# Kernel tuning notes

Measured on AMD Instinct MI355X. Metric: run time of the kernel, lower is better.

Reference implementation:

```python
import math
import jax, jax.numpy as jnp
import numpy as np

DIM_IN = 2048
DIM_OUT = 2048
BLOCK = 128
N_BLOCKS = 256
SPARSITY = 0.1
BATCH = 8192


def setup_inputs() -> dict:
    key = jax.random.key(0)
    k1, k2, k3, k4, k5 = jax.random.split(key, 5)
    x = jax.random.normal(k1, (BATCH, DIM_IN), dtype=jnp.float32)
    weight = jax.random.normal(k2, (DIM_IN, DIM_OUT), dtype=jnp.float32) * (1.0 / math.sqrt(DIM_IN))
    bias = jax.random.normal(k3, (DIM_OUT,), dtype=jnp.float32) * 0.01
    gate_w = jax.random.normal(k4, (DIM_IN, N_BLOCKS), dtype=jnp.float32) * (1.0 / math.sqrt(DIM_IN))
    gate_b = jax.random.normal(k5, (N_BLOCKS,), dtype=jnp.float32) * 0.01
    return {"x": x, "weight": weight, "bias": bias, "gate_w": gate_w, "gate_b": gate_b}


def _sparsify1d(g):
    # k-th largest kept per row; threshold, mask, renormalize (Sparsify1D)
    n = g.shape[-1]
    k = int(math.ceil(SPARSITY * n))
    topval = jax.lax.top_k(g, k)[0][:, -1:]          # (B, 1) k-th largest value
    res = jnp.where(g >= topval, g, jnp.zeros_like(g))
    return res / (jnp.sum(res, axis=-1, keepdims=True) / n)


def reference(x, weight, bias, gate_w, gate_b):
    B = x.shape[0]
    s = DIM_IN // BLOCK                               # 16 block-rows/cols
    # gate network: Linear -> Sparsify1D
    g = _sparsify1d(x @ gate_w + gate_b)              # (B, s*s)
    gb = g.reshape(B, s, s)                           # (B, s_in, s_out)
    xb = x.reshape(B, s, BLOCK)                       # (B, s_in, block)
    Wb = weight.reshape(s, BLOCK, s, BLOCK)           # (s_in, block, s_out, block)
    # gated block matrix-vector multiply:
    # y[b,q,n] = sum_{p,m} g[b,p,q] * x[b,p,m] * W[p,m,q,n]
    y = jnp.einsum('bpq,bpm,pmqn->bqn', gb, xb, Wb)
    return y.reshape(B, DIM_OUT) + bias
```

## Files before the change

kernel.cpp:

```cpp
#include <hip/hip_runtime.h>
#include <hip/hip_bf16.h>
#include <stdint.h>

#define BATCH  8192
#define DIN    2048
#define DOUT   2048
#define NB     256
#define KSEL   26

typedef __attribute__((ext_vector_type(2))) float f32x2;
typedef __attribute__((ext_vector_type(4))) float f32x4;
typedef __attribute__((ext_vector_type(8))) __bf16 bf16x8;
typedef __attribute__((ext_vector_type(8))) unsigned short u16x8;
typedef __attribute__((ext_vector_type(4))) unsigned short u16x4;

__device__ __forceinline__ float bf2f(unsigned short u){
  union { unsigned int i; float f; } v; v.i = ((unsigned int)u) << 16; return v.f;
}
__device__ __forceinline__ unsigned short f2bf(float f){
  union { float f; unsigned int i; } v; v.f = f;
  unsigned int x = v.i;
  return (unsigned short)((x + 0x7FFFu + ((x >> 16) & 1u)) >> 16);
}
__device__ __forceinline__ unsigned short f2bf_c(float f){
  __bf16 b = (__bf16)f;
  union { __bf16 b; unsigned short u; } v; v.b = b; return v.u;
}

__global__ __launch_bounds__(256) void conv_wt(const float* __restrict__ w, unsigned short* __restrict__ wt)
{
  __shared__ float tl[64][65];
  const int k0 = blockIdx.x * 64;
  const int n0 = blockIdx.y * 64;
  const int c  = threadIdx.x & 63;
  const int r4 = threadIdx.x >> 6;
  #pragma unroll
  for (int i = 0; i < 16; i++){
    const int r = r4 * 16 + i;
    tl[r][c] = w[(size_t)(k0 + r) * DOUT + n0 + c];
  }
  __syncthreads();
  #pragma unroll
  for (int i = 0; i < 16; i++){
    const int n = r4 * 16 + i;
    wt[(size_t)(n0 + n) * DIN + k0 + c] = f2bf(tl[c][n]);
  }
}

__global__ __launch_bounds__(256) void gate_gemm(
    const float* __restrict__ x, const float* __restrict__ gw,
    float* __restrict__ part, unsigned short* __restrict__ xb)
{
  __shared__ float xT[32][36];
  const int b0   = blockIdx.x * 32;
  const int ks   = blockIdx.y;
  const int t    = threadIdx.x;
  const int lane = t & 63;
  const int wv   = t >> 6;
  const int rg   = (wv >> 1) * 16;
  const int cb   = (wv & 1) * 128 + (lane << 1);

  float acc[16][2];
  #pragma unroll
  for (int i = 0; i < 16; i++){ acc[i][0] = 0.f; acc[i][1] = 0.f; }

  const int sr = t >> 3;
  const int sk = (t & 7) * 4;

  const int koff = ks * 1024;
  for (int kc = 0; kc < 1024; kc += 32){
    __syncthreads();
    {
      const size_t gi = (size_t)(b0 + sr) * DIN + koff + kc + sk;
      f32x4 a = *(const f32x4*)&x[gi];
      u16x4 ob;
      #pragma unroll
      for (int j = 0; j < 4; j++) ob[j] = f2bf_c(a[j]);
      *(u16x4*)&xb[gi] = ob;
      #pragma unroll
      for (int j = 0; j < 4; j++) xT[sk + j][sr] = a[j];
    }
    __syncthreads();
    const float* gwp = &gw[(size_t)(koff + kc) * NB + cb];
    #pragma unroll 4
    for (int k = 0; k < 32; k++){
      f32x2 wvv = *(const f32x2*)(gwp + (size_t)k * NB);
      f32x4 xv0 = *(const f32x4*)&xT[k][rg];
      f32x4 xv1 = *(const f32x4*)&xT[k][rg + 4];
      f32x4 xv2 = *(const f32x4*)&xT[k][rg + 8];
      f32x4 xv3 = *(const f32x4*)&xT[k][rg + 12];
      #pragma unroll
      for (int j = 0; j < 4; j++){
        acc[j][0]      = fmaf(xv0[j], wvv[0], acc[j][0]);
        acc[j][1]      = fmaf(xv0[j], wvv[1], acc[j][1]);
        acc[j + 4][0]  = fmaf(xv1[j], wvv[0], acc[j + 4][0]);
        acc[j + 4][1]  = fmaf(xv1[j], wvv[1], acc[j + 4][1]);
        acc[j + 8][0]  = fmaf(xv2[j], wvv[0], acc[j + 8][0]);
        acc[j + 8][1]  = fmaf(xv2[j], wvv[1], acc[j + 8][1]);
        acc[j + 12][0] = fmaf(xv3[j], wvv[0], acc[j + 12][0]);
        acc[j + 12][1] = fmaf(xv3[j], wvv[1], acc[j + 12][1]);
      }
    }
  }
  float* dst = part + (size_t)ks * BATCH * NB;
  #pragma unroll
  for (int i = 0; i < 16; i++){
    const int row = b0 + rg + i;
    f32x2 o; o[0] = acc[i][0]; o[1] = acc[i][1];
    *(f32x2*)&dst[(size_t)row * NB + cb] = o;
  }
}

__global__ __launch_bounds__(256) void topk(float* __restrict__ part, const float* __restrict__ gb)
{
  const int lane = threadIdx.x & 63;
  const int row  = blockIdx.x * 4 + (threadIdx.x >> 6);
  f32x4* p0 = (f32x4*)&part[(size_t)row * NB];
  const f32x4* p1 = (const f32x4*)&part[(size_t)(BATCH + row) * NB];
  const f32x4* gbv = (const f32x4*)gb;
  f32x4 v = p0[lane] + p1[lane] + gbv[lane];

  const float NEG = -3.402823466e38f;
  float w0 = v[0], w1 = v[1], w2 = v[2], w3 = v[3];
  float thr = 0.f;
  for (int it = 0; it < KSEL; it++){
    float lm = fmaxf(fmaxf(w0, w1), fmaxf(w2, w3));
    float wm = lm;
    #pragma unroll
    for (int off = 32; off; off >>= 1) wm = fmaxf(wm, __shfl_xor(wm, off, 64));
    unsigned long long ball = __ballot(lm == wm);
    int first = __ffsll(ball) - 1;
    if (lane == first){
      if      (w0 == wm) w0 = NEG;
      else if (w1 == wm) w1 = NEG;
      else if (w2 == wm) w2 = NEG;
      else               w3 = NEG;
    }
    thr = wm;
  }
  float s = 0.f;
  #pragma unroll
  for (int j = 0; j < 4; j++) s += (v[j] >= thr) ? v[j] : 0.f;
  #pragma unroll
  for (int off = 32; off; off >>= 1) s += __shfl_xor(s, off, 64);
  const float d = s * (1.0f / NB);
  f32x4 o;
  #pragma unroll
  for (int j = 0; j < 4; j++) o[j] = (v[j] >= thr) ? v[j] / d : 0.f;
  p0[lane] = o;
}

__global__ __launch_bounds__(256) void main_gemm(
    const unsigned short* __restrict__ xb,
    const unsigned short* __restrict__ wt,
    const float* __restrict__ g,
    const float* __restrict__ bias,
    float* __restrict__ out)
{
  __shared__ unsigned short xa[128][72];
  __shared__ unsigned short wb[128][72];
  __shared__ float gl[128 * 17];

  const int q    = blockIdx.x;
  const int b0   = blockIdx.y * 128;
  const int t    = threadIdx.x;
  const int lane = t & 63;
  const int wid  = t >> 6;
  const int wr   = (wid >> 1) * 64;
  const int wc   = (wid & 1) * 64;
  const int l15  = lane & 15;
  const int l4   = lane >> 4;

  for (int e = t; e < 128 * 16; e += 256){
    const int r = e >> 4, p = e & 15;
    gl[r * 17 + p] = g[(size_t)(b0 + r) * NB + p * 16 + q];
  }

  f32x4 acc[4][4];
  #pragma unroll
  for (int m = 0; m < 4; m++)
    #pragma unroll
    for (int n = 0; n < 4; n++) acc[m][n] = (f32x4)0.0f;

  const int row_s = t >> 1;
  const int half  = t & 1;

  for (int kp = 0; kp < 32; kp++){
    const int p = kp >> 1;
    __syncthreads();
    {
      const float gate = gl[row_s * 17 + p];
      const unsigned short* src = &xb[(size_t)(b0 + row_s) * DIN + kp * 64 + half * 32];
      unsigned short* dst = &xa[row_s][half * 32];
      #pragma unroll
      for (int c = 0; c < 4; c++){
        u16x8 u = *(const u16x8*)(src + c * 8);
        u16x8 o;
        #pragma unroll
        for (int j = 0; j < 8; j++) o[j] = f2bf_c(bf2f(u[j]) * gate);
        *(u16x8*)(dst + c * 8) = o;
      }
    }
    {
      const unsigned short* src = &wt[(size_t)(q * 128 + row_s) * DIN + kp * 64 + half * 32];
      unsigned short* dst = &wb[row_s][half * 32];
      #pragma unroll
      for (int c = 0; c < 4; c++)
        *(u16x8*)(dst + c * 8) = *(const u16x8*)(src + c * 8);
    }
    __syncthreads();
    #pragma unroll
    for (int ksi = 0; ksi < 2; ksi++){
      const int kk = ksi * 32 + l4 * 8;
      bf16x8 a[4], b[4];
      #pragma unroll
      for (int m = 0; m < 4; m++)
        a[m] = *(const bf16x8*)&xa[wr + m * 16 + l15][kk];
      #pragma unroll
      for (int n = 0; n < 4; n++)
        b[n] = *(const bf16x8*)&wb[wc + n * 16 + l15][kk];
      #pragma unroll
      for (int m = 0; m < 4; m++)
        #pragma unroll
        for (int n = 0; n < 4; n++)
          acc[m][n] = __builtin_amdgcn_mfma_f32_16x16x32_bf16(a[m], b[n], acc[m][n], 0, 0, 0);
    }
  }

  #pragma unroll
  for (int n = 0; n < 4; n++){
    const int col = q * 128 + wc + n * 16 + l15;
    const float bv = bias[col];
    #pragma unroll
    for (int m = 0; m < 4; m++){
      #pragma unroll
      for (int r = 0; r < 4; r++){
        const int row = b0 + wr + m * 16 + l4 * 4 + r;
        out[(size_t)row * DOUT + col] = acc[m][n][r] + bv;
      }
    }
  }
}

extern "C" void kernel_launch(void* const* d_in, const int* in_sizes, int n_in,
                              void* d_out, int out_size, void* d_ws, size_t ws_size,
                              hipStream_t stream)
{
  const float* x    = (const float*)d_in[0];
  const float* w    = (const float*)d_in[1];
  const float* bias = (const float*)d_in[2];
  const float* gw   = (const float*)d_in[3];
  const float* gb   = (const float*)d_in[4];
  float* out = (float*)d_out;

  float*          part = (float*)d_ws;
  unsigned short* wtb  = (unsigned short*)((char*)d_ws + (size_t)16 * 1024 * 1024);
  unsigned short* xbb  = (unsigned short*)((char*)d_ws + (size_t)24 * 1024 * 1024);

  conv_wt  <<<dim3(DIN / 64, DOUT / 64), 256, 0, stream>>>(w, wtb);
  gate_gemm<<<dim3(BATCH / 32, 2), 256, 0, stream>>>(x, gw, part, xbb);
  topk     <<<BATCH / 4, 256, 0, stream>>>(part, gb);
  main_gemm<<<dim3(16, BATCH / 128), 256, 0, stream>>>(xbb, wtb, part, bias, out);
}
```

Measured before the change: 312.9 us.

## Restructure gate GEMM to read x directly via broadcast loads, dropping LDS staging

The gate GEMM kernel no longer stages a transposed x tile in shared memory with two barriers per chunk. Each thread now computes an 8-row by 4-column tile, loading x rows straight from global memory (all lanes in a wave read the same address, so the load is a broadcast) and gate weights as float4. The bf16 copy of x is written by one selected lane per row. This removes LDS traffic and barriers, but leans on cache broadcast for the x loads, and the bf16 stores now go through a divergent branch.

```diff
diff --git a/kernel.cpp b/kernel.cpp
--- a/kernel.cpp
+++ b/kernel.cpp
@@ -51,64 +51,55 @@
     const float* __restrict__ x, const float* __restrict__ gw,
     float* __restrict__ part, unsigned short* __restrict__ xb)
 {
-  __shared__ float xT[32][36];
   const int b0   = blockIdx.x * 32;
   const int ks   = blockIdx.y;
   const int t    = threadIdx.x;
-  const int lane = t & 63;
-  const int wv   = t >> 6;
-  const int rg   = (wv >> 1) * 16;
-  const int cb   = (wv & 1) * 128 + (lane << 1);
-
-  float acc[16][2];
-  #pragma unroll
-  for (int i = 0; i < 16; i++){ acc[i][0] = 0.f; acc[i][1] = 0.f; }
-
-  const int sr = t >> 3;
-  const int sk = (t & 7) * 4;
-
+  const int ct   = t & 63;
+  const int rt   = t >> 6;
+  const int row0 = b0 + rt * 8;
   const int koff = ks * 1024;
-  for (int kc = 0; kc < 1024; kc += 32){
-    __syncthreads();
-    {
-      const size_t gi = (size_t)(b0 + sr) * DIN + koff + kc + sk;
-      f32x4 a = *(const f32x4*)&x[gi];
-      u16x4 ob;
-      #pragma unroll
-      for (int j = 0; j < 4; j++) ob[j] = f2bf_c(a[j]);
-      *(u16x4*)&xb[gi] = ob;
-      #pragma unroll
-      for (int j = 0; j < 4; j++) xT[sk + j][sr] = a[j];
-    }
-    __syncthreads();
-    const float* gwp = &gw[(size_t)(koff + kc) * NB + cb];
-    #pragma unroll 4
-    for (int k = 0; k < 32; k++){
-      f32x2 wvv = *(const f32x2*)(gwp + (size_t)k * NB);
-      f32x4 xv0 = *(const f32x4*)&xT[k][rg];
-      f32x4 xv1 = *(const f32x4*)&xT[k][rg + 4];
-      f32x4 xv2 = *(const f32x4*)&xT[k][rg + 8];
-      f32x4 xv3 = *(const f32x4*)&xT[k][rg + 12];
-      #pragma unroll
-      for (int j = 0; j < 4; j++){
-        acc[j][0]      = fmaf(xv0[j], wvv[0], acc[j][0]);
-        acc[j][1]      = fmaf(xv0[j], wvv[1], acc[j][1]);
-        acc[j + 4][0]  = fmaf(xv1[j], wvv[0], acc[j + 4][0]);
-        acc[j + 4][1]  = fmaf(xv1[j], wvv[1], acc[j + 4][1]);
-        acc[j + 8][0]  = fmaf(xv2[j], wvv[0], acc[j + 8][0]);
-        acc[j + 8][1]  = fmaf(xv2[j], wvv[1], acc[j + 8][1]);
-        acc[j + 12][0] = fmaf(xv3[j], wvv[0], acc[j + 12][0]);
-        acc[j + 12][1] = fmaf(xv3[j], wvv[1], acc[j + 12][1]);
-      }
-    }
-  }
+
+  f32x4 acc[8];
+  #pragma unroll
+  for (int r = 0; r < 8; r++) acc[r] = (f32x4)0.0f;
+
+  const float* xp = x  + (size_t)row0 * DIN + koff;
+  const float* wp = gw + (size_t)koff * NB + ct * 4;
+
+  for (int kc = 0; kc < 1024; kc += 8){
+    f32x4 xv[8][2];
+    #pragma unroll
+    for (int r = 0; r < 8; r++){
+      xv[r][0] = *(const f32x4*)(xp + (size_t)r * DIN + kc);
+      xv[r][1] = *(const f32x4*)(xp + (size_t)r * DIN + kc + 4);
+    }
+    #pragma unroll
+    for (int j = 0; j < 8; j++){
+      f32x4 wv = *(const f32x4*)(wp + (size_t)(kc + j) * NB);
+      #pragma unroll
+      for (int r = 0; r < 8; r++){
+        const float xr = xv[r][j >> 2][j & 3];
+        acc[r][0] = fmaf(xr, wv[0], acc[r][0]);
+        acc[r][1] = fmaf(xr, wv[1], acc[r][1]);
+        acc[r][2] = fmaf(xr, wv[2], acc[r][2]);
+        acc[r][3] = fmaf(xr, wv[3], acc[r][3]);
+      }
+    }
+    #pragma unroll
+    for (int r = 0; r < 8; r++){
+      if (ct == r){
+        u16x8 o;
+        #pragma unroll
+        for (int j = 0; j < 8; j++) o[j] = f2bf_c(xv[r][j >> 2][j & 3]);
+        *(u16x8*)&xb[(size_t)(row0 + r) * DIN + koff + kc] = o;
+      }
+    }
+  }
+
   float* dst = part + (size_t)ks * BATCH * NB;
   #pragma unroll
-  for (int i = 0; i < 16; i++){
-    const int row = b0 + rg + i;
-    f32x2 o; o[0] = acc[i][0]; o[1] = acc[i][1];
-    *(f32x2*)&dst[(size_t)row * NB + cb] = o;
-  }
+  for (int r = 0; r < 8; r++)
+    *(f32x4*)&dst[(size_t)(row0 + r) * NB + ct * 4] = acc[r];
 }
 
 __global__ __launch_bounds__(256) void topk(float* __restrict__ part, const float* __restrict__ gb)
```

After: 340.9 us. +9.0%, slower.

## Compute gate GEMM with split-bf16 MFMA and refine near-tie rows in fp32

Applied to the files above, without the earlier changes.

Replaces the scalar fp32 gate GEMM, which ran as two K-split halves, with a single-pass MFMA kernel. Both x and the gate weights are split into bf16 hi and lo parts and combined with three MFMAs per tile (bf16x3) to approximate fp32 accuracy, using double-buffered LDS staging. Top-k now also finds the 27th value and flags rows where the 26th and 27th values are within a small delta; a refine kernel recomputes those rows' gate logits exactly in fp32 and redoes the selection. The change adds a gate-weight conversion kernel and an extra launch, and correctness on ties depends on the chosen delta.

```diff
diff --git a/kernel.cpp b/kernel.cpp
--- a/kernel.cpp
+++ b/kernel.cpp
@@ -7,9 +7,11 @@
 #define DOUT   2048
 #define NB     256
 #define KSEL   26
+#define GDELTA 1e-4f
 
 typedef __attribute__((ext_vector_type(2))) float f32x2;
 typedef __attribute__((ext_vector_type(4))) float f32x4;
+typedef __attribute__((ext_vector_type(16))) float f32x16;
 typedef __attribute__((ext_vector_type(8))) __bf16 bf16x8;
 typedef __attribute__((ext_vector_type(8))) unsigned short u16x8;
 typedef __attribute__((ext_vector_type(4))) unsigned short u16x4;
@@ -47,83 +49,130 @@
   }
 }
 
-__global__ __launch_bounds__(256) void gate_gemm(
-    const float* __restrict__ x, const float* __restrict__ gw,
-    float* __restrict__ part, unsigned short* __restrict__ xb)
-{
-  __shared__ float xT[32][36];
+__global__ __launch_bounds__(256) void conv_gwt(const float* __restrict__ gw,
+    unsigned short* __restrict__ ghiT, unsigned short* __restrict__ gloT)
+{
+  __shared__ float tl[64][65];
+  const int k0 = blockIdx.x * 64;
+  const int n0 = blockIdx.y * 64;
+  const int c  = threadIdx.x & 63;
+  const int r4 = threadIdx.x >> 6;
+  #pragma unroll
+  for (int i = 0; i < 16; i++){
+    const int r = r4 * 16 + i;
+    tl[r][c] = gw[(size_t)(k0 + r) * NB + n0 + c];
+  }
+  __syncthreads();
+  #pragma unroll
+  for (int i = 0; i < 16; i++){
+    const int n = r4 * 16 + i;
+    const float v = tl[c][n];
+    const unsigned short h = f2bf_c(v);
+    ghiT[(size_t)(n0 + n) * DIN + k0 + c] = h;
+    gloT[(size_t)(n0 + n) * DIN + k0 + c] = f2bf_c(v - bf2f(h));
+  }
+}
+
+__global__ __launch_bounds__(256) void gate_mfma(
+    const float* __restrict__ x,
+    const unsigned short* __restrict__ ghiT,
+    const unsigned short* __restrict__ gloT,
+    float* __restrict__ part,
+    unsigned short* __restrict__ xb)
+{
+  __shared__ unsigned short Ah[2][32][40], Al[2][32][40];
+  __shared__ unsigned short Bh[2][256][40], Bl[2][256][40];
+
   const int b0   = blockIdx.x * 32;
-  const int ks   = blockIdx.y;
   const int t    = threadIdx.x;
   const int lane = t & 63;
   const int wv   = t >> 6;
-  const int rg   = (wv >> 1) * 16;
-  const int cb   = (wv & 1) * 128 + (lane << 1);
-
-  float acc[16][2];
-  #pragma unroll
-  for (int i = 0; i < 16; i++){ acc[i][0] = 0.f; acc[i][1] = 0.f; }
+  const int l31  = lane & 31;
+  const int lk   = (lane >> 5) * 8;
 
   const int sr = t >> 3;
   const int sk = (t & 7) * 4;
-
-  const int koff = ks * 1024;
-  for (int kc = 0; kc < 1024; kc += 32){
+  const int bc = t >> 2;
+  const int bk = (t & 3) * 8;
+
+  f32x16 acc[2];
+  acc[0] = (f32x16)0.f; acc[1] = (f32x16)0.f;
+
+  auto STAGE = [&](int bb, int k0){
+    f32x4 a = *(const f32x4*)&x[(size_t)(b0 + sr) * DIN + k0 + sk];
+    u16x4 hi4, lo4;
+    #pragma unroll
+    for (int j = 0; j < 4; j++){
+      const unsigned short h = f2bf_c(a[j]);
+      hi4[j] = h;
+      lo4[j] = f2bf_c(a[j] - bf2f(h));
+    }
+    *(u16x4*)&Ah[bb][sr][sk] = hi4;
+    *(u16x4*)&Al[bb][sr][sk] = lo4;
+    *(u16x4*)&xb[(size_t)(b0 + sr) * DIN + k0 + sk] = hi4;
+    #pragma unroll
+    for (int p = 0; p < 4; p++){
+      const int col = bc + p * 64;
+      u16x8 vh = *(const u16x8*)&ghiT[(size_t)col * DIN + k0 + bk];
+      *(u16x8*)&Bh[bb][col][bk] = vh;
+      u16x8 vl = *(const u16x8*)&gloT[(size_t)col * DIN + k0 + bk];
+      *(u16x8*)&Bl[bb][col][bk] = vl;
+    }
+  };
+
+  STAGE(0, 0);
+  __syncthreads();
+  int cur = 0;
+  for (int ks = 0; ks < 64; ks++){
+    if (ks < 63) STAGE(cur ^ 1, (ks + 1) * 32);
+    bf16x8 ah[2], al[2], bh[2][2], bl[2][2];
+    #pragma unroll
+    for (int kh = 0; kh < 2; kh++){
+      const int ko = kh * 16 + lk;
+      ah[kh] = *(const bf16x8*)&Ah[cur][l31][ko];
+      al[kh] = *(const bf16x8*)&Al[cur][l31][ko];
+      #pragma unroll
+      for (int n = 0; n < 2; n++){
+        bh[n][kh] = *(const bf16x8*)&Bh[cur][wv * 64 + n * 32 + l31][ko];
+        bl[n][kh] = *(const bf16x8*)&Bl[cur][wv * 64 + n * 32 + l31][ko];
+      }
+    }
+    #pragma unroll
+    for (int n = 0; n < 2; n++)
+      #pragma unroll
+      for (int kh = 0; kh < 2; kh++){
+        acc[n] = __builtin_amdgcn_mfma_f32_32x32x16_bf16(ah[kh], bh[n][kh], acc[n], 0, 0, 0);
+        acc[n] = __builtin_amdgcn_mfma_f32_32x32x16_bf16(ah[kh], bl[n][kh], acc[n], 0, 0, 0);
+        acc[n] = __builtin_amdgcn_mfma_f32_32x32x16_bf16(al[kh], bh[n][kh], acc[n], 0, 0, 0);
+      }
     __syncthreads();
-    {
-      const size_t gi = (size_t)(b0 + sr) * DIN + koff + kc + sk;
-      f32x4 a = *(const f32x4*)&x[gi];
-      u16x4 ob;
-      #pragma unroll
-      for (int j = 0; j < 4; j++) ob[j] = f2bf_c(a[j]);
-      *(u16x4*)&xb[gi] = ob;
-      #pragma unroll
-      for (int j = 0; j < 4; j++) xT[sk + j][sr] = a[j];
-    }
-    __syncthreads();
-    const float* gwp = &gw[(size_t)(koff + kc) * NB + cb];
-    #pragma unroll 4
-    for (int k = 0; k < 32; k++){
-      f32x2 wvv = *(const f32x2*)(gwp + (size_t)k * NB);
-      f32x4 xv0 = *(const f32x4*)&xT[k][rg];
-      f32x4 xv1 = *(const f32x4*)&xT[k][rg + 4];
-      f32x4 xv2 = *(const f32x4*)&xT[k][rg + 8];
-      f32x4 xv3 = *(const f32x4*)&xT[k][rg + 12];
-      #pragma unroll
-      for (int j = 0; j < 4; j++){
-        acc[j][0]      = fmaf(xv0[j], wvv[0], acc[j][0]);
-        acc[j][1]      = fmaf(xv0[j], wvv[1], acc[j][1]);
-        acc[j + 4][0]  = fmaf(xv1[j], wvv[0], acc[j + 4][0]);
-        acc[j + 4][1]  = fmaf(xv1[j], wvv[1], acc[j + 4][1]);
-        acc[j + 8][0]  = fmaf(xv2[j], wvv[0], acc[j + 8][0]);
-        acc[j + 8][1]  = fmaf(xv2[j], wvv[1], acc[j + 8][1]);
-        acc[j + 12][0] = fmaf(xv3[j], wvv[0], acc[j + 12][0]);
-        acc[j + 12][1] = fmaf(xv3[j], wvv[1], acc[j + 12][1]);
-      }
-    }
-  }
-  float* dst = part + (size_t)ks * BATCH * NB;
-  #pragma unroll
-  for (int i = 0; i < 16; i++){
-    const int row = b0 + rg + i;
-    f32x2 o; o[0] = acc[i][0]; o[1] = acc[i][1];
-    *(f32x2*)&dst[(size_t)row * NB + cb] = o;
-  }
-}
-
-__global__ __launch_bounds__(256) void topk(float* __restrict__ part, const float* __restrict__ gb)
+    cur ^= 1;
+  }
+
+  #pragma unroll
+  for (int n = 0; n < 2; n++){
+    const int col = wv * 64 + n * 32 + l31;
+    #pragma unroll
+    for (int r = 0; r < 16; r++){
+      const int row = (r & 3) + 8 * (r >> 2) + 4 * (lane >> 5);
+      part[(size_t)(b0 + row) * NB + col] = acc[n][r];
+    }
+  }
+}
+
+__global__ __launch_bounds__(256) void topk(float* __restrict__ part,
+    const float* __restrict__ gb, int* __restrict__ flags)
 {
   const int lane = threadIdx.x & 63;
   const int row  = blockIdx.x * 4 + (threadIdx.x >> 6);
   f32x4* p0 = (f32x4*)&part[(size_t)row * NB];
-  const f32x4* p1 = (const f32x4*)&part[(size_t)(BATCH + row) * NB];
   const f32x4* gbv = (const f32x4*)gb;
-  f32x4 v = p0[lane] + p1[lane] + gbv[lane];
+  f32x4 v = p0[lane] + gbv[lane];
 
   const float NEG = -3.402823466e38f;
   float w0 = v[0], w1 = v[1], w2 = v[2], w3 = v[3];
-  float thr = 0.f;
-  for (int it = 0; it < KSEL; it++){
+  float thr = 0.f, nxt = 0.f;
+  for (int it = 0; it < KSEL + 1; it++){
     float lm = fmaxf(fmaxf(w0, w1), fmaxf(w2, w3));
     float wm = lm;
     #pragma unroll
@@ -136,8 +185,10 @@
       else if (w2 == wm) w2 = NEG;
       else               w3 = NEG;
     }
-    thr = wm;
-  }
+    if (it < KSEL) thr = wm; else nxt = wm;
+  }
+  if (lane == 0) flags[row] = (thr - nxt < GDELTA) ? 1 : 0;
+
   float s = 0.f;
   #pragma unroll
   for (int j = 0; j < 4; j++) s += (v[j] >= thr) ? v[j] : 0.f;
@@ -148,6 +199,66 @@
   #pragma unroll
   for (int j = 0; j < 4; j++) o[j] = (v[j] >= thr) ? v[j] / d : 0.f;
   p0[lane] = o;
+}
+
+__global__ __launch_bounds__(256) void refine(
+    const float* __restrict__ x, const float* __restrict__ gw,
+    const float* __restrict__ gb, const int* __restrict__ flags,
+    float* __restrict__ part)
+{
+  const int lane = threadIdx.x & 63;
+  const int row  = blockIdx.x * 4 + (threadIdx.x >> 6);
+  if (!flags[row]) return;
+
+  f32x4 acc0 = (f32x4)0.f, acc1 = (f32x4)0.f;
+  const float* xp = &x[(size_t)row * DIN];
+  #pragma unroll 8
+  for (int k = 0; k < 1024; k++){
+    const float xv = xp[k];
+    const f32x4 wv = *(const f32x4*)&gw[(size_t)k * NB + lane * 4];
+    #pragma unroll
+    for (int j = 0; j < 4; j++) acc0[j] = fmaf(xv, wv[j], acc0[j]);
+  }
+  #pragma unroll 8
+  for (int k = 1024; k < 2048; k++){
+    const float xv = xp[k];
+    const f32x4 wv = *(const f32x4*)&gw[(size_t)k * NB + lane * 4];
+    #pragma unroll
+    for (int j = 0; j < 4; j++) acc1[j] = fmaf(xv, wv[j], acc1[j]);
+  }
+  const f32x4 gbv = *(const f32x4*)&gb[lane * 4];
+  f32x4 v;
+  #pragma unroll
+  for (int j = 0; j < 4; j++) v[j] = acc0[j] + acc1[j] + gbv[j];
+
+  const float NEG = -3.402823466e38f;
+  float w0 = v[0], w1 = v[1], w2 = v[2], w3 = v[3];
+  float thr = 0.f;
+  for (int it = 0; it < KSEL; it++){
+    float lm = fmaxf(fmaxf(w0, w1), fmaxf(w2, w3));
+    float wm = lm;
+    #pragma unroll
+    for (int off = 32; off; off >>= 1) wm = fmaxf(wm, __shfl_xor(wm, off, 64));
+    unsigned long long ball = __ballot(lm == wm);
+    int first = __ffsll(ball) - 1;
+    if (lane == first){
+      if      (w0 == wm) w0 = NEG;
+      else if (w1 == wm) w1 = NEG;
+      else if (w2 == wm) w2 = NEG;
+      else               w3 = NEG;
+    }
+    thr = wm;
+  }
+  float s = 0.f;
+  #pragma unroll
+  for (int j = 0; j < 4; j++) s += (v[j] >= thr) ? v[j] : 0.f;
+  #pragma unroll
+  for (int off = 32; off; off >>= 1) s += __shfl_xor(s, off, 64);
+  const float d = s * (1.0f / NB);
+  f32x4 o;
+  #pragma unroll
+  for (int j = 0; j < 4; j++) o[j] = (v[j] >= thr) ? v[j] / d : 0.f;
+  *(f32x4*)&part[(size_t)row * NB + lane * 4] = o;
 }
 
 __global__ __launch_bounds__(256) void main_gemm(
@@ -253,12 +364,18 @@
   const float* gb   = (const float*)d_in[4];
   float* out = (float*)d_out;
 
-  float*          part = (float*)d_ws;
-  unsigned short* wtb  = (unsigned short*)((char*)d_ws + (size_t)16 * 1024 * 1024);
-  unsigned short* xbb  = (unsigned short*)((char*)d_ws + (size_t)24 * 1024 * 1024);
+  char* wsb = (char*)d_ws;
+  float*          part = (float*)wsb;
+  unsigned short* wtb  = (unsigned short*)(wsb + (size_t)8  * 1024 * 1024);
+  unsigned short* xbb  = (unsigned short*)(wsb + (size_t)16 * 1024 * 1024);
+  unsigned short* ghiT = (unsigned short*)(wsb + (size_t)48 * 1024 * 1024);
+  unsigned short* gloT = (unsigned short*)(wsb + (size_t)49 * 1024 * 1024);
+  int*            flg  = (int*)           (wsb + (size_t)50 * 1024 * 1024);
 
   conv_wt  <<<dim3(DIN / 64, DOUT / 64), 256, 0, stream>>>(w, wtb);
-  gate_gemm<<<dim3(BATCH / 32, 2), 256, 0, stream>>>(x, gw, part, xbb);
-  topk     <<<BATCH / 4, 256, 0, stream>>>(part, gb);
+  conv_gwt <<<dim3(DIN / 64, NB / 64),   256, 0, stream>>>(gw, ghiT, gloT);
+  gate_mfma<<<BATCH / 32, 256, 0, stream>>>(x, ghiT, gloT, part, xbb);
+  topk     <<<BATCH / 4, 256, 0, stream>>>(part, gb, flg);
+  refine   <<<BATCH / 4, 256, 0, stream>>>(x, gw, gb, flg, part);
   main_gemm<<<dim3(16, BATCH / 128), 256, 0, stream>>>(xbb, wtb, part, bias, out);
 }
```

New measurement: 305.5 us. 2.4% less time.
